# Performance work log

Measured on AMD Instinct MI355X. Metric: run time of the kernel, lower is better.

The kernel has to match this reference:

```python
import jax, jax.numpy as jnp
import numpy as np

DIM = 256
HEADS = 8
GROUPS = 4
HIDDEN = int(DIM * 4.0)
GW = DIM // GROUPS          # group width = 64
HEAD_DIM = DIM // HEADS     # 32
SCALE = HEAD_DIM ** (-0.5)
LN_EPS = 1e-6
BN_EPS = 1e-3               # keras BatchNormalization default epsilon
L2_EPS = 1e-12              # tf.nn.l2_normalize default


def _l2norm(t):
    ss = jnp.sum(t * t, axis=-1, keepdims=True)
    return t * jax.lax.rsqrt(jnp.maximum(ss, L2_EPS))


def setup_inputs() -> dict:
    key = jax.random.key(0)
    ks = jax.random.split(key, 12)
    B, H, W = 16, 56, 56
    x = jax.random.normal(ks[0], (B, H, W, DIM), jnp.float32)
    # depthwise 3x3 kernels for groups 1..GROUPS-1 (group 0's conv is unused in the
    # original code: y0 is a plain slice). Combined depthwise kernel over the last
    # (GROUPS-1)*GW channels, keras HWIO layout with in_ch_per_group = 1.
    dw_kernel = jax.random.normal(ks[1], (3, 3, 1, (GROUPS - 1) * GW), jnp.float32) * 0.05
    dw_bias = jnp.zeros(((GROUPS - 1) * GW,), jnp.float32)
    ln_gamma = jnp.ones((DIM,), jnp.float32)
    ln_beta = jnp.zeros((DIM,), jnp.float32)
    qkv_w = jax.random.normal(ks[2], (DIM, 3 * DIM), jnp.float32) * 0.02  # qkv_bias=False
    proj_w = jax.random.normal(ks[3], (DIM, DIM), jnp.float32) * 0.02
    proj_b = jnp.zeros((DIM,), jnp.float32)
    bn_gamma = jnp.ones((DIM,), jnp.float32)
    bn_beta = jnp.zeros((DIM,), jnp.float32)
    bn_mean = jax.random.normal(ks[4], (DIM,), jnp.float32) * 0.1
    bn_var = jax.random.uniform(ks[5], (DIM,), jnp.float32, 0.5, 1.5)
    fc1_w = jax.random.normal(ks[6], (DIM, HIDDEN), jnp.float32) * 0.02
    fc1_b = jnp.zeros((HIDDEN,), jnp.float32)
    fc2_w = jax.random.normal(ks[7], (HIDDEN, DIM), jnp.float32) * 0.02
    fc2_b = jnp.zeros((DIM,), jnp.float32)
    return dict(x=x, dw_kernel=dw_kernel, dw_bias=dw_bias, ln_gamma=ln_gamma,
                ln_beta=ln_beta, qkv_w=qkv_w, proj_w=proj_w, proj_b=proj_b,
                bn_gamma=bn_gamma, bn_beta=bn_beta, bn_mean=bn_mean, bn_var=bn_var,
                fc1_w=fc1_w, fc1_b=fc1_b, fc2_w=fc2_w, fc2_b=fc2_b)


def _gdta_forward(x, dw_kernel, dw_bias, ln_gamma, ln_beta, qkv_w, proj_w, proj_b,
                  bn_gamma, bn_beta, bn_mean, bn_var, fc1_w, fc1_b, fc2_w, fc2_b):
    B, H, W, C = x.shape
    N = H * W
    # ---- GOTA_block_part1: grouped depthwise convs with cumulative residual ----
    # y0 = x[..., :GW]; for i>=1: K_i = dwconv_i(x_i); y1=K1, y_i = K_i + y_{i-1}
    # => y_i (i>=1) is the cumulative sum of K_1..K_i along the group axis.
    xc = x[..., GW:]  # [B,H,W,(G-1)*GW]
    K = jax.lax.conv_general_dilated(
        xc, dw_kernel, window_strides=(1, 1), padding='SAME',
        dimension_numbers=('NHWC', 'HWIO', 'NHWC'),
        feature_group_count=(GROUPS - 1) * GW) + dw_bias
    Kg = K.reshape(B, H, W, GROUPS - 1, GW)
    Yg = jnp.cumsum(Kg, axis=3).reshape(B, H, W, (GROUPS - 1) * GW)
    dwconv = jnp.concatenate([x[..., :GW], Yg], axis=-1)  # [B,H,W,C]
    # ---- LayerNorm (last axis) ----
    mu = jnp.mean(dwconv, axis=-1, keepdims=True)
    var = jnp.mean(jnp.square(dwconv - mu), axis=-1, keepdims=True)
    norm1 = (dwconv - mu) * jax.lax.rsqrt(var + LN_EPS) * ln_gamma + ln_beta
    t = norm1.reshape(B, N, C)
    # ---- channel (cross-covariance) attention ----
    qkv = (t @ qkv_w).reshape(B, N, 3, HEADS, HEAD_DIM)
    qkv = jnp.transpose(qkv, (2, 0, 3, 1, 4))  # [3,B,h,N,d]
    q, k, v = qkv[0], qkv[1], qkv[2]
    q = _l2norm(q) * SCALE
    k = _l2norm(k)
    attn = jnp.einsum('bhnd,bhne->bhde', q, k)       # [B,h,d,d]
    attn = jax.nn.softmax(attn, axis=-1)
    out = jnp.einsum('bhnd,bhde->bhne', v, attn)     # [B,h,N,d]
    out = jnp.transpose(out, (0, 2, 1, 3)).reshape(B, N, C)
    out = out @ proj_w + proj_b
    attn_img = out.reshape(B, H, W, C)
    # ---- merge + BatchNorm (inference) + MLP + residual ----
    merged = attn_img + dwconv
    merged = (merged - bn_mean) * jax.lax.rsqrt(bn_var + BN_EPS) * bn_gamma + bn_beta
    h1 = jax.nn.gelu(merged @ fc1_w + fc1_b, approximate=False)
    mlp = h1 @ fc2_w + fc2_b
    return x + mlp


def reference(x, dw_kernel, dw_bias, ln_gamma, ln_beta, qkv_w, proj_w, proj_b,
              bn_gamma, bn_beta, bn_mean, bn_var, fc1_w, fc1_b, fc2_w, fc2_b):
    return _gdta_forward(x, dw_kernel, dw_bias, ln_gamma, ln_beta, qkv_w, proj_w,
                         proj_b, bn_gamma, bn_beta, bn_mean, bn_var,
                         fc1_w, fc1_b, fc2_w, fc2_b)
```

## Files before the change

kernel.cpp:

```cpp
#include <hip/hip_runtime.h>
#include <cstdint>

typedef unsigned short u16;
typedef __attribute__((ext_vector_type(8))) _Float16 f16x8;
typedef __attribute__((ext_vector_type(8))) unsigned short u16x8;
typedef __attribute__((ext_vector_type(4))) float f32x4;

#define SPLITN 7

__device__ __forceinline__ float b2f(u16 u) {
  union { unsigned int i; float f; } v; v.i = ((unsigned int)u) << 16; return v.f;
}
__device__ __forceinline__ u16 f2b(float f) {
  union { float f; unsigned int i; } v; v.f = f;
  unsigned int x = v.i;
  return (u16)((x + 0x7fffu + ((x >> 16) & 1u)) >> 16);
}
__device__ __forceinline__ u16 f2h(float f) {
  union { _Float16 h; u16 u; } v; v.h = (_Float16)f; return v.u;
}
__device__ __forceinline__ float h2f(u16 u) {
  union { u16 u; _Float16 h; } v; v.u = u; return (float)v.h;
}
__device__ __forceinline__ float ld(const void* p, long i, int f) {
  return f ? ((const float*)p)[i] : b2f(((const u16*)p)[i]);
}
template<int F>
__device__ __forceinline__ float4 ld4(const void* p, long i) {
  if (F) return *(const float4*)((const float*)p + i);
  const ushort4 u = *(const ushort4*)((const u16*)p + i);
  return make_float4(b2f(u.x), b2f(u.y), b2f(u.z), b2f(u.w));
}
__device__ __forceinline__ void fma4(float4& a, const float4 x, const float4 k) {
  a.x += x.x * k.x; a.y += x.y * k.y; a.z += x.z * k.z; a.w += x.w * k.w;
}
__device__ __forceinline__ float gelu(float v) {
  const float u = v * (0.7978845608028654f + 0.035677408136300125f * v * v);
  const float e = __expf(2.0f * u);
  return 0.5f * v * (1.0f + (1.0f - 2.0f / (e + 1.0f)));
}
#define GLDS(gp, lp) __builtin_amdgcn_global_load_lds( \
    (const __attribute__((address_space(1))) void*)(gp), \
    (__attribute__((address_space(3))) void*)(lp), 16, 0, 0)

__global__ __launch_bounds__(256) void detect_kernel(const u16* __restrict__ x,
                                                     int* __restrict__ flag) {
  __shared__ int sbad;
  if (threadIdx.x == 0) sbad = 0;
  __syncthreads();
  int b = 0;
  #pragma unroll
  for (int rr = 0; rr < 2; ++rr) {
    const int i = rr * 256 + threadIdx.x;
    const float v = fabsf(b2f(x[2 * i]));
    if (!(v < 100.f) || v < 1e-6f) ++b;
  }
  atomicAdd(&sbad, b);
  __syncthreads();
  if (threadIdx.x == 0) *flag = (sbad > 16) ? 1 : 0;
}

__global__ void transpose_cvt_kernel(const void* __restrict__ w0, u16* __restrict__ o0,
                                     const void* __restrict__ w1, u16* __restrict__ o1,
                                     const void* __restrict__ w2, u16* __restrict__ o2,
                                     const int* __restrict__ flagp) {
  const int f = *flagp;
  int bb = blockIdx.x;
  const void* in; u16* out; int R, C;
  if (bb < 768)       { in = w0; out = o0; R = 256;  C = 768;  }
  else if (bb < 1792) { in = w1; out = o1; R = 256;  C = 1024; bb -= 768; }
  else                { in = w2; out = o2; R = 1024; C = 256;  bb -= 1792; }
  const int o = bb * 256 + threadIdx.x;
  if (o < R * C) {
    const int i = o / R, j = o % R;
    out[o] = f2h(ld(in, (long)j * C + i, f));
  }
}

template<int F>
__device__ __forceinline__ void dwconv_body4(
    const void* __restrict__ x, const void* __restrict__ dwk, const void* __restrict__ dwb,
    const void* __restrict__ lng, const void* __restrict__ lnb,
    u16* __restrict__ dwc, u16* __restrict__ norm1, int tg, int lane)
{
  const int b = tg / 784, rem = tg % 784;
  const int hh = rem / 14, wg = (rem % 14) * 4;
  const int c0 = lane * 4;
  const long tok0 = (long)b * 3136 + hh * 56 + wg;
  float4 acc[4];
  float4 pv[4];
  if (lane >= 16) {
    const int j0 = c0 - 64;
    const float4 bb = ld4<F>(dwb, j0);
    acc[0] = bb; acc[1] = bb; acc[2] = bb; acc[3] = bb;
    #pragma unroll
    for (int dh = -1; dh <= 1; ++dh) {
      const int h2 = hh + dh;
      if (h2 < 0 || h2 >= 56) continue;
      const long rb = ((long)b * 3136 + h2 * 56) * 256;
      float4 xr[6];
      #pragma unroll
      for (int i = 0; i < 6; ++i) {
        const int w2 = wg - 1 + i;
        xr[i] = (w2 >= 0 && w2 < 56) ? ld4<F>(x, rb + (long)w2 * 256 + c0)
                                     : make_float4(0.f, 0.f, 0.f, 0.f);
      }
      float4 kw[3];
      #pragma unroll
      for (int i = 0; i < 3; ++i)
        kw[i] = ld4<F>(dwk, (long)((dh + 1) * 3 + i) * 192 + j0);
      #pragma unroll
      for (int t = 0; t < 4; ++t)
        #pragma unroll
        for (int i = 0; i < 3; ++i)
          fma4(acc[t], xr[t + i], kw[i]);
    }
  } else {
    #pragma unroll
    for (int t = 0; t < 4; ++t)
      pv[t] = ld4<F>(x, (tok0 + t) * 256 + c0);
  }
  const float4 g = ld4<F>(lng, c0);
  const float4 be = ld4<F>(lnb, c0);
  #pragma unroll
  for (int t = 0; t < 4; ++t) {
    float sx = acc[t].x, sy = acc[t].y, sz = acc[t].z, sw = acc[t].w;
    const float t1x = __shfl(sx, lane - 16), t1y = __shfl(sy, lane - 16),
                t1z = __shfl(sz, lane - 16), t1w = __shfl(sw, lane - 16);
    const float t2x = __shfl(sx, lane - 32), t2y = __shfl(sy, lane - 32),
                t2z = __shfl(sz, lane - 32), t2w = __shfl(sw, lane - 32);
    if (lane >= 32) { sx += t1x; sy += t1y; sz += t1z; sw += t1w; }
    if (lane >= 48) { sx += t2x; sy += t2y; sz += t2z; sw += t2w; }
    float vx, vy, vz, vw;
    if (lane < 16) { vx = pv[t].x; vy = pv[t].y; vz = pv[t].z; vw = pv[t].w; }
    else           { vx = sx;      vy = sy;      vz = sz;      vw = sw;      }
    float sum = vx + vy + vz + vw;
    float sq = vx * vx + vy * vy + vz * vz + vw * vw;
    #pragma unroll
    for (int m = 32; m; m >>= 1) { sum += __shfl_xor(sum, m); sq += __shfl_xor(sq, m); }
    const float mu = sum * (1.0f / 256.0f);
    const float var = sq * (1.0f / 256.0f) - mu * mu;
    const float rstd = rsqrtf(fmaxf(var, 0.f) + 1e-6f);
    ushort4 dv, nv;
    dv.x = f2h(vx); dv.y = f2h(vy); dv.z = f2h(vz); dv.w = f2h(vw);
    nv.x = f2h((vx - mu) * rstd * g.x + be.x);
    nv.y = f2h((vy - mu) * rstd * g.y + be.y);
    nv.z = f2h((vz - mu) * rstd * g.z + be.z);
    nv.w = f2h((vw - mu) * rstd * g.w + be.w);
    *(ushort4*)(dwc + (tok0 + t) * 256 + c0) = dv;
    *(ushort4*)(norm1 + (tok0 + t) * 256 + c0) = nv;
  }
}

__global__ __launch_bounds__(256) void dwconv_ln_kernel(
    const void* __restrict__ x, const void* __restrict__ dwk, const void* __restrict__ dwb,
    const void* __restrict__ lng, const void* __restrict__ lnb,
    u16* __restrict__ dwc, u16* __restrict__ norm1, const int* __restrict__ flagp)
{
  const int wave = threadIdx.x >> 6, lane = threadIdx.x & 63;
  const int tg = blockIdx.x * 4 + wave;
  if (*flagp) dwconv_body4<1>(x, dwk, dwb, lng, lnb, dwc, norm1, tg, lane);
  else        dwconv_body4<0>(x, dwk, dwb, lng, lnb, dwc, norm1, tg, lane);
}

template<int BM, int WR, int WC, int EPI, int KT>
__global__ __launch_bounds__(256) void gemm_kernel(
    const u16* __restrict__ A, const u16* __restrict__ Bt, void* C,
    int lda, int ldb, int ldc,
    long aZ, long bZ, long cZ, long zoff,
    const void* __restrict__ bias, const void* aux,
    const void* __restrict__ bng, const void* __restrict__ bnb,
    const void* __restrict__ bnm, const void* __restrict__ bnv,
    const int* __restrict__ flagp)
{
  static_assert(BM == 64 || BM == 128, "");
  constexpr int BN = 128;
  constexpr int WM = BM / WR, WN = BN / WC;
  constexpr int MI = WM / 16, NI = WN / 16;
  __shared__ __align__(16) u16 As[BM * 64];
  __shared__ __align__(16) u16 Bs[BN * 64];
  const int f = (EPI == 0 || EPI == 5) ? 0 : *flagp;
  const int tid = threadIdx.x;
  const int wave = tid >> 6, lane = tid & 63;
  const int wr = wave / WC, wc = wave % WC;
  const int quad = lane >> 4, l16 = lane & 15;
  const int tileM = blockIdx.y * BM, tileN = blockIdx.x * BN;
  const u16* Ab = A + (long)blockIdx.z * aZ + (long)tileM * lda;
  const u16* Bb = Bt + (long)blockIdx.z * bZ + (long)tileN * ldb;
  f32x4 acc[MI][NI];
  #pragma unroll
  for (int mi = 0; mi < MI; ++mi)
    #pragma unroll
    for (int ni = 0; ni < NI; ++ni)
      acc[mi][ni] = (f32x4){0.f, 0.f, 0.f, 0.f};

  for (int k0 = 0; k0 < KT; k0 += 64) {
    #pragma unroll
    for (int r = 0; r < BM / 32; ++r) {
      const int fg = r * 256 + tid;
      const int row = fg >> 3, cs = (fg & 7) ^ (row & 7);
      GLDS(Ab + (long)row * lda + k0 + cs * 8, As + (r * 256 + wave * 64) * 8);
    }
    #pragma unroll
    for (int r = 0; r < 4; ++r) {
      const int fg = r * 256 + tid;
      const int row = fg >> 3, cs = (fg & 7) ^ (row & 7);
      GLDS(Bb + (long)row * ldb + k0 + cs * 8, Bs + (r * 256 + wave * 64) * 8);
    }
    __syncthreads();
    #pragma unroll
    for (int ks = 0; ks < 2; ++ks) {
      f16x8 af[MI], bfr[NI];
      #pragma unroll
      for (int mi = 0; mi < MI; ++mi) {
        const int R = wr * WM + mi * 16 + l16;
        const int kc = ks * 4 + quad;
        af[mi] = *(const f16x8*)&As[(R * 8 + (kc ^ (R & 7))) * 8];
      }
      #pragma unroll
      for (int ni = 0; ni < NI; ++ni) {
        const int S = wc * WN + ni * 16 + l16;
        const int kc = ks * 4 + quad;
        bfr[ni] = *(const f16x8*)&Bs[(S * 8 + (kc ^ (S & 7))) * 8];
      }
      #pragma unroll
      for (int mi = 0; mi < MI; ++mi)
        #pragma unroll
        for (int ni = 0; ni < NI; ++ni)
          acc[mi][ni] = __builtin_amdgcn_mfma_f32_16x16x32_f16(af[mi], bfr[ni], acc[mi][ni], 0, 0, 0);
    }
    __syncthreads();
  }

  const long zC = (long)blockIdx.z * cZ + ((EPI == 5) ? 0 : zoff);
  #pragma unroll
  for (int mi = 0; mi < MI; ++mi) {
    #pragma unroll
    for (int ni = 0; ni < NI; ++ni) {
      const int col = tileN + wc * WN + ni * 16 + l16;
      #pragma unroll
      for (int r = 0; r < 4; ++r) {
        const int row = tileM + wr * WM + mi * 16 + quad * 4 + r;
        const long ci = zC + (long)row * ldc + col;
        float v = acc[mi][ni][r];
        if (EPI == 2) {
          v += ld(bias, col, f);
          v += h2f(((const u16*)aux)[ci]);
          v = (v - ld(bnm, col, f)) * rsqrtf(ld(bnv, col, f) + 1e-3f) * ld(bng, col, f) + ld(bnb, col, f);
          ((u16*)C)[ci] = f2h(v);
        } else {
          if (col < 512) ((u16*)C)[(long)row * 512 + col] = f2h(v);
          else ((u16*)aux)[zoff + (long)row * 256 + (col - 512)] = f2h(v);
        }
      }
    }
  }
}

__global__ __launch_bounds__(256, 2) void mlp_kernel(
    const u16* __restrict__ dwc, const u16* __restrict__ w1t, const u16* __restrict__ w2t,
    const void* __restrict__ b1, const void* __restrict__ b2,
    const void* __restrict__ x, void* __restrict__ out,
    const int* __restrict__ flagp)
{
  __shared__ __align__(16) u16 Ds[64 * 256];
  __shared__ __align__(16) u16 Hs[64 * 128];
  __shared__ __align__(16) u16 Bs[256 * 64];
  const int f = *flagp;
  const int tid = threadIdx.x;
  const int wave = tid >> 6, lane = tid & 63;
  const int quad = lane >> 4, l16 = lane & 15;
  const int tileM = blockIdx.x * 64;

  #pragma unroll
  for (int r = 0; r < 8; ++r) {
    const int fg = r * 256 + tid;
    const int row = fg >> 5, cs = (fg & 31) ^ (row & 7);
    GLDS(dwc + (long)(tileM + row) * 256 + cs * 8, Ds + (r * 256 + wave * 64) * 8);
  }

  f32x4 accO[4][4];
  #pragma unroll
  for (int mi = 0; mi < 4; ++mi)
    #pragma unroll
    for (int ni = 0; ni < 4; ++ni)
      accO[mi][ni] = (f32x4){0.f, 0.f, 0.f, 0.f};

  for (int hc = 0; hc < 8; ++hc) {
    f32x4 acc1[4][2];
    #pragma unroll
    for (int mi = 0; mi < 4; ++mi)
      #pragma unroll
      for (int ni = 0; ni < 2; ++ni)
        acc1[mi][ni] = (f32x4){0.f, 0.f, 0.f, 0.f};

    for (int it = 0; it < 4; ++it) {
      #pragma unroll
      for (int r = 0; r < 4; ++r) {
        const int fg = r * 256 + tid;
        const int row = fg >> 3, cs = (fg & 7) ^ (row & 7);
        GLDS(w1t + (long)(hc * 128 + row) * 256 + it * 64 + cs * 8,
             Bs + (r * 256 + wave * 64) * 8);
      }
      __syncthreads();
      #pragma unroll
      for (int ks = 0; ks < 2; ++ks) {
        const int kc = it * 8 + ks * 4 + quad;
        const int kl = ks * 4 + quad;
        f16x8 af[4], bf[2];
        #pragma unroll
        for (int mi = 0; mi < 4; ++mi) {
          const int R = mi * 16 + l16;
          af[mi] = *(const f16x8*)&Ds[(R * 32 + (kc ^ (R & 7))) * 8];
        }
        #pragma unroll
        for (int ni = 0; ni < 2; ++ni) {
          const int S = wave * 32 + ni * 16 + l16;
          bf[ni] = *(const f16x8*)&Bs[(S * 8 + (kl ^ (S & 7))) * 8];
        }
        #pragma unroll
        for (int mi = 0; mi < 4; ++mi)
          #pragma unroll
          for (int ni = 0; ni < 2; ++ni)
            acc1[mi][ni] = __builtin_amdgcn_mfma_f32_16x16x32_f16(af[mi], bf[ni], acc1[mi][ni], 0, 0, 0);
      }
      __syncthreads();
    }
    #pragma unroll
    for (int mi = 0; mi < 4; ++mi)
      #pragma unroll
      for (int ni = 0; ni < 2; ++ni)
        #pragma unroll
        for (int r = 0; r < 4; ++r) {
          const int row = mi * 16 + quad * 4 + r;
          const int col = wave * 32 + ni * 16 + l16;
          const float v = acc1[mi][ni][r] + ld(b1, hc * 128 + col, f);
          Hs[(row * 16 + ((col >> 3) ^ (row & 7))) * 8 + (col & 7)] = f2h(gelu(v));
        }
    __syncthreads();
    for (int it2 = 0; it2 < 2; ++it2) {
      #pragma unroll
      for (int r = 0; r < 8; ++r) {
        const int fg = r * 256 + tid;
        const int row = fg >> 3, cs = (fg & 7) ^ (row & 7);
        GLDS(w2t + (long)row * 1024 + hc * 128 + it2 * 64 + cs * 8,
             Bs + (r * 256 + wave * 64) * 8);
      }
      __syncthreads();
      #pragma unroll
      for (int ks = 0; ks < 2; ++ks) {
        const int kc = it2 * 8 + ks * 4 + quad;
        const int kl = ks * 4 + quad;
        f16x8 af[4], bf[4];
        #pragma unroll
        for (int mi = 0; mi < 4; ++mi) {
          const int R = mi * 16 + l16;
          af[mi] = *(const f16x8*)&Hs[(R * 16 + (kc ^ (R & 7))) * 8];
        }
        #pragma unroll
        for (int ni = 0; ni < 4; ++ni) {
          const int S = wave * 64 + ni * 16 + l16;
          bf[ni] = *(const f16x8*)&Bs[(S * 8 + (kl ^ (S & 7))) * 8];
        }
        #pragma unroll
        for (int mi = 0; mi < 4; ++mi)
          #pragma unroll
          for (int ni = 0; ni < 4; ++ni)
            accO[mi][ni] = __builtin_amdgcn_mfma_f32_16x16x32_f16(af[mi], bf[ni], accO[mi][ni], 0, 0, 0);
      }
      __syncthreads();
    }
  }
  #pragma unroll
  for (int mi = 0; mi < 4; ++mi)
    #pragma unroll
    for (int ni = 0; ni < 4; ++ni) {
      const int col = wave * 64 + ni * 16 + l16;
      #pragma unroll
      for (int r = 0; r < 4; ++r) {
        const int row = tileM + mi * 16 + quad * 4 + r;
        const long ci = (long)row * 256 + col;
        const float v = accO[mi][ni][r] + ld(b2, col, f) + ld(x, ci, f);
        if (f) ((float*)out)[ci] = v; else ((u16*)out)[ci] = f2b(v);
      }
    }
}

__global__ __launch_bounds__(256) void attn_accum_kernel(
    const u16* __restrict__ qk, float* __restrict__ A_part, int pair0)
{
  const int pl = blockIdx.x;
  const int split = blockIdx.y;
  const int bl = pl >> 3, h = pl & 7;
  const int tid = threadIdx.x;
  const int wave = tid >> 6, lane = tid & 63;
  const int quad = lane >> 4, l16 = lane & 15;
  const int dq = wave >> 1, eq = wave & 1;
  __shared__ __align__(16) u16 lqT[32 * 72];
  __shared__ __align__(16) u16 lkT[32 * 72];
  const long rowbase = (long)bl * 3136 * 512;
  const int n0 = split * 448;
  f32x4 acc = (f32x4){0.f, 0.f, 0.f, 0.f};
  const int seg = tid & 7;

  for (int ch = 0; ch < 7; ++ch) {
    const int nb = n0 + ch * 64;
    #pragma unroll
    for (int rr = 0; rr < 2; ++rr) {
      const int a = rr * 256 + tid;
      const int nl = a >> 3;
      const int co = (seg < 4) ? h * 32 + seg * 8 : 256 + h * 32 + (seg - 4) * 8;
      const u16x8 v8 = *(const u16x8*)(qk + rowbase + (long)(nb + nl) * 512 + co);
      float vf[8], p = 0.f;
      #pragma unroll
      for (int i = 0; i < 8; ++i) { vf[i] = h2f(v8[i]); p += vf[i] * vf[i]; }
      float p1 = p + __shfl_xor(p, 1);
      float p2 = p1 + __shfl_xor(p1, 2);
      const float other = __shfl_xor(p2, 4);
      const float ssq = (seg < 4) ? p2 : other;
      const float ssk = (seg < 4) ? other : p2;
      const float s = 0.17677669529663687f * rsqrtf(fmaxf(ssq, 1e-12f)) *
                      rsqrtf(fmaxf(ssk, 1e-12f));
      if (seg < 4) {
        const int db = seg * 8;
        #pragma unroll
        for (int i = 0; i < 8; ++i) {
          const int d = db + i;
          lqT[d * 72 + (nl ^ (d & 24))] = f2h(vf[i] * s);
        }
      } else {
        const int eb = (seg - 4) * 8;
        #pragma unroll
        for (int i = 0; i < 8; ++i) {
          const int e = eb + i;
          lkT[e * 72 + (nl ^ (e & 24))] = v8[i];
        }
      }
    }
    __syncthreads();
    #pragma unroll
    for (int ks = 0; ks < 2; ++ks) {
      const int tb = ks * 32 + quad * 8;
      const int dA = dq * 16 + l16;
      const int eB = eq * 16 + l16;
      const f16x8 af = *(const f16x8*)&lqT[dA * 72 + (tb ^ (dA & 24))];
      const f16x8 bf = *(const f16x8*)&lkT[eB * 72 + (tb ^ (eB & 24))];
      acc = __builtin_amdgcn_mfma_f32_16x16x32_f16(af, bf, acc, 0, 0, 0);
    }
    __syncthreads();
  }
  float* o = A_part + ((long)(pair0 + pl) * SPLITN + split) * 1024;
  #pragma unroll
  for (int r = 0; r < 4; ++r)
    o[(dq * 16 + quad * 4 + r) * 32 + eq * 16 + l16] = acc[r];
}

__global__ __launch_bounds__(1024) void softmax_kernel(float* A_part) {
  const int pair = blockIdx.x;
  const int t = threadIdx.x;
  float v = 0.f;
  float* base = A_part + (long)pair * SPLITN * 1024 + t;
  #pragma unroll
  for (int s = 0; s < SPLITN; ++s) v += base[s * 1024];
  float mx = v;
  #pragma unroll
  for (int m = 16; m; m >>= 1) mx = fmaxf(mx, __shfl_xor(mx, m, 32));
  const float p = expf(v - mx);
  float sm = p;
  #pragma unroll
  for (int m = 16; m; m >>= 1) sm += __shfl_xor(sm, m, 32);
  base[0] = p / sm;
}

__global__ __launch_bounds__(256) void wb_kernel(
    const float* __restrict__ A_part, const void* __restrict__ proj_w,
    u16* __restrict__ Wbt, const int* __restrict__ flagp)
{
  const int f = *flagp;
  const int b = blockIdx.x;
  const int cs = blockIdx.y;
  const int tid = threadIdx.x;
  const int cg = tid & 31, dg = tid >> 5;
  const int c = cs * 32 + cg;
  __shared__ float Ah[32][32];
  __shared__ float pw[32][33];
  for (int h = 0; h < 8; ++h) {
    const float* Abase = A_part + ((long)(b * 8 + h) * SPLITN) * 1024;
    #pragma unroll
    for (int rr = 0; rr < 4; ++rr) {
      const int ff = rr * 256 + tid;
      Ah[ff >> 5][ff & 31] = Abase[ff];
    }
    #pragma unroll
    for (int rr = 0; rr < 4; ++rr) {
      const int ff = rr * 256 + tid;
      const int e = ff >> 5, ccc = ff & 31;
      pw[e][ccc] = ld(proj_w, (long)(h * 32 + e) * 256 + cs * 32 + ccc, f);
    }
    __syncthreads();
    float acc[4] = {0.f, 0.f, 0.f, 0.f};
    #pragma unroll
    for (int e = 0; e < 32; ++e) {
      const float pv = pw[e][cg];
      #pragma unroll
      for (int dd = 0; dd < 4; ++dd)
        acc[dd] += Ah[dg * 4 + dd][e] * pv;
    }
    #pragma unroll
    for (int dd = 0; dd < 4; ++dd)
      Wbt[((long)b * 256 + c) * 256 + h * 32 + dg * 4 + dd] = f2h(acc[dd]);
    __syncthreads();
  }
}

extern "C" void kernel_launch(void* const* d_in, const int* in_sizes, int n_in,
                              void* d_out, int out_size, void* d_ws, size_t ws_size,
                              hipStream_t stream) {
  const void* x      = d_in[0];
  const void* dwk    = d_in[1];
  const void* dwb    = d_in[2];
  const void* lng    = d_in[3];
  const void* lnb    = d_in[4];
  const void* qkv_w  = d_in[5];
  const void* proj_w = d_in[6];
  const void* proj_b = d_in[7];
  const void* bn_g   = d_in[8];
  const void* bn_b   = d_in[9];
  const void* bn_m   = d_in[10];
  const void* bn_v   = d_in[11];
  const void* fc1_w  = d_in[12];
  const void* fc1_b  = d_in[13];
  const void* fc2_w  = d_in[14];
  const void* fc2_b  = d_in[15];
  char* ws = (char*)d_ws;

  int*   flagp   = (int*)  (ws + 0);
  u16*   wqkvT   = (u16*)  (ws + 256);
  u16*   wfc1T   = (u16*)  (ws + 393472);
  u16*   wfc2T   = (u16*)  (ws + 917760);
  float* A_part  = (float*)(ws + 1442048);
  u16*   Wbt     = (u16*)  (ws + 5112064);
  u16*   vbuf    = (u16*)  (ws + 7209216);
  u16*   dwc     = (u16*)  (ws + 32899328);
  u16*   qk_half = (u16*)  (ws + 58589440);
  u16*   norm1   = (u16*)d_out;

  detect_kernel<<<1, 256, 0, stream>>>((const u16*)x, flagp);

  transpose_cvt_kernel<<<2816, 256, 0, stream>>>(qkv_w, wqkvT, fc1_w, wfc1T,
                                                 fc2_w, wfc2T, flagp);

  dwconv_ln_kernel<<<3136, 256, 0, stream>>>(x, dwk, dwb, lng, lnb, dwc, norm1, flagp);

  for (int half = 0; half < 2; ++half) {
    const u16* nh = norm1 + (long)half * 25088 * 256;
    gemm_kernel<128, 2, 2, 5, 256><<<dim3(6, 196, 1), 256, 0, stream>>>(
        nh, wqkvT, qk_half, 256, 256, 512, 0, 0, 0, (long)half * 25088 * 256,
        nullptr, vbuf, nullptr, nullptr, nullptr, nullptr, flagp);
    attn_accum_kernel<<<dim3(64, SPLITN), 256, 0, stream>>>(qk_half, A_part, half * 64);
  }

  softmax_kernel<<<128, 1024, 0, stream>>>(A_part);
  wb_kernel<<<dim3(16, 8), 256, 0, stream>>>(A_part, proj_w, Wbt, flagp);

  gemm_kernel<64, 1, 4, 2, 256><<<dim3(2, 49, 16), 256, 0, stream>>>(
      vbuf, Wbt, dwc, 256, 256, 256,
      (long)3136 * 256, 65536, (long)3136 * 256, 0,
      proj_b, dwc, bn_g, bn_b, bn_m, bn_v, flagp);

  mlp_kernel<<<784, 256, 0, stream>>>(dwc, wfc1T, wfc2T, fc1_b, fc2_b, x, d_out, flagp);
}
```

Baseline: 464.1 us.

## Read weight fragments directly from global memory instead of staging in LDS

Both the QKV/proj GEMMs and the fused MLP now keep only the activation tile in shared memory and load B-operand (weight) fragments straight from global memory/L2 into registers, removing the per-k-step weight staging and most __syncthreads. The GEMM uses a 64-row tile with full K resident in LDS and a 2x2 wave layout. The MLP switches to a 2x2 wave layout, drops the weight LDS buffer and uses a padded hidden buffer, allowing higher occupancy. The risk is uncoalesced, latency-bound global weight reads that rely on cache hits.

```diff
diff --git a/kernel.cpp b/kernel.cpp
--- a/kernel.cpp
+++ b/kernel.cpp
@@ -163,113 +163,98 @@
   else        dwconv_body4<0>(x, dwk, dwb, lng, lnb, dwc, norm1, tg, lane);
 }
 
-template<int BM, int WR, int WC, int EPI, int KT>
-__global__ __launch_bounds__(256) void gemm_kernel(
+template<int EPI>
+__global__ __launch_bounds__(256, 4) void sgemm_kernel(
     const u16* __restrict__ A, const u16* __restrict__ Bt, void* C,
-    int lda, int ldb, int ldc,
-    long aZ, long bZ, long cZ, long zoff,
+    int ldb, long aZ, long bZ, long cZ, long zoff,
     const void* __restrict__ bias, const void* aux,
     const void* __restrict__ bng, const void* __restrict__ bnb,
     const void* __restrict__ bnm, const void* __restrict__ bnv,
     const int* __restrict__ flagp)
 {
-  static_assert(BM == 64 || BM == 128, "");
-  constexpr int BN = 128;
-  constexpr int WM = BM / WR, WN = BN / WC;
-  constexpr int MI = WM / 16, NI = WN / 16;
-  __shared__ __align__(16) u16 As[BM * 64];
-  __shared__ __align__(16) u16 Bs[BN * 64];
-  const int f = (EPI == 0 || EPI == 5) ? 0 : *flagp;
+  __shared__ __align__(16) u16 Ds[64 * 256];
+  const int f = (EPI == 5) ? 0 : *flagp;
   const int tid = threadIdx.x;
   const int wave = tid >> 6, lane = tid & 63;
-  const int wr = wave / WC, wc = wave % WC;
   const int quad = lane >> 4, l16 = lane & 15;
-  const int tileM = blockIdx.y * BM, tileN = blockIdx.x * BN;
-  const u16* Ab = A + (long)blockIdx.z * aZ + (long)tileM * lda;
-  const u16* Bb = Bt + (long)blockIdx.z * bZ + (long)tileN * ldb;
-  f32x4 acc[MI][NI];
-  #pragma unroll
-  for (int mi = 0; mi < MI; ++mi)
-    #pragma unroll
-    for (int ni = 0; ni < NI; ++ni)
+  const int wr = wave >> 1, wc = wave & 1;
+  const int tileM = blockIdx.y * 64, colC = blockIdx.x * 128;
+  const u16* Ab = A + (long)blockIdx.z * aZ + (long)tileM * 256;
+  const u16* Bb = Bt + (long)blockIdx.z * bZ;
+
+  #pragma unroll
+  for (int r = 0; r < 8; ++r) {
+    const int fg = r * 256 + tid;
+    const int row = fg >> 5, cs = (fg & 31) ^ (row & 7);
+    GLDS(Ab + (long)row * 256 + cs * 8, Ds + (r * 256 + wave * 64) * 8);
+  }
+  __syncthreads();
+
+  f32x4 acc[2][4];
+  #pragma unroll
+  for (int mi = 0; mi < 2; ++mi)
+    #pragma unroll
+    for (int ni = 0; ni < 4; ++ni)
       acc[mi][ni] = (f32x4){0.f, 0.f, 0.f, 0.f};
 
-  for (int k0 = 0; k0 < KT; k0 += 64) {
-    #pragma unroll
-    for (int r = 0; r < BM / 32; ++r) {
-      const int fg = r * 256 + tid;
-      const int row = fg >> 3, cs = (fg & 7) ^ (row & 7);
-      GLDS(Ab + (long)row * lda + k0 + cs * 8, As + (r * 256 + wave * 64) * 8);
-    }
-    #pragma unroll
-    for (int r = 0; r < 4; ++r) {
-      const int fg = r * 256 + tid;
-      const int row = fg >> 3, cs = (fg & 7) ^ (row & 7);
-      GLDS(Bb + (long)row * ldb + k0 + cs * 8, Bs + (r * 256 + wave * 64) * 8);
-    }
-    __syncthreads();
-    #pragma unroll
-    for (int ks = 0; ks < 2; ++ks) {
-      f16x8 af[MI], bfr[NI];
-      #pragma unroll
-      for (int mi = 0; mi < MI; ++mi) {
-        const int R = wr * WM + mi * 16 + l16;
-        const int kc = ks * 4 + quad;
-        af[mi] = *(const f16x8*)&As[(R * 8 + (kc ^ (R & 7))) * 8];
-      }
-      #pragma unroll
-      for (int ni = 0; ni < NI; ++ni) {
-        const int S = wc * WN + ni * 16 + l16;
-        const int kc = ks * 4 + quad;
-        bfr[ni] = *(const f16x8*)&Bs[(S * 8 + (kc ^ (S & 7))) * 8];
-      }
-      #pragma unroll
-      for (int mi = 0; mi < MI; ++mi)
-        #pragma unroll
-        for (int ni = 0; ni < NI; ++ni)
-          acc[mi][ni] = __builtin_amdgcn_mfma_f32_16x16x32_f16(af[mi], bfr[ni], acc[mi][ni], 0, 0, 0);
-    }
-    __syncthreads();
-  }
-
-  const long zC = (long)blockIdx.z * cZ + ((EPI == 5) ? 0 : zoff);
-  #pragma unroll
-  for (int mi = 0; mi < MI; ++mi) {
-    #pragma unroll
-    for (int ni = 0; ni < NI; ++ni) {
-      const int col = tileN + wc * WN + ni * 16 + l16;
+  #pragma unroll
+  for (int kk = 0; kk < 8; ++kk) {
+    const int kc = kk * 4 + quad;
+    f16x8 af[2], bf[4];
+    #pragma unroll
+    for (int mi = 0; mi < 2; ++mi) {
+      const int R = wr * 32 + mi * 16 + l16;
+      af[mi] = *(const f16x8*)&Ds[(R * 32 + (kc ^ (R & 7))) * 8];
+    }
+    #pragma unroll
+    for (int ni = 0; ni < 4; ++ni) {
+      const int S = colC + wc * 64 + ni * 16 + l16;
+      bf[ni] = *(const f16x8*)(Bb + (long)S * ldb + kc * 8);
+    }
+    #pragma unroll
+    for (int mi = 0; mi < 2; ++mi)
+      #pragma unroll
+      for (int ni = 0; ni < 4; ++ni)
+        acc[mi][ni] = __builtin_amdgcn_mfma_f32_16x16x32_f16(af[mi], bf[ni], acc[mi][ni], 0, 0, 0);
+  }
+
+  #pragma unroll
+  for (int mi = 0; mi < 2; ++mi)
+    #pragma unroll
+    for (int ni = 0; ni < 4; ++ni) {
+      const int col = colC + wc * 64 + ni * 16 + l16;
       #pragma unroll
       for (int r = 0; r < 4; ++r) {
-        const int row = tileM + wr * WM + mi * 16 + quad * 4 + r;
-        const long ci = zC + (long)row * ldc + col;
+        const int rloc = wr * 32 + mi * 16 + quad * 4 + r;
         float v = acc[mi][ni][r];
         if (EPI == 2) {
+          const long ci = (long)blockIdx.z * cZ + (long)(tileM + rloc) * 256 + col;
           v += ld(bias, col, f);
           v += h2f(((const u16*)aux)[ci]);
           v = (v - ld(bnm, col, f)) * rsqrtf(ld(bnv, col, f) + 1e-3f) * ld(bng, col, f) + ld(bnb, col, f);
           ((u16*)C)[ci] = f2h(v);
         } else {
-          if (col < 512) ((u16*)C)[(long)row * 512 + col] = f2h(v);
-          else ((u16*)aux)[zoff + (long)row * 256 + (col - 512)] = f2h(v);
+          const long row = tileM + rloc;
+          if (col < 512) ((u16*)C)[row * 512 + col] = f2h(v);
+          else ((u16*)aux)[zoff + row * 256 + (col - 512)] = f2h(v);
         }
       }
     }
-  }
-}
-
-__global__ __launch_bounds__(256, 2) void mlp_kernel(
+}
+
+__global__ __launch_bounds__(256, 3) void mlp_kernel(
     const u16* __restrict__ dwc, const u16* __restrict__ w1t, const u16* __restrict__ w2t,
     const void* __restrict__ b1, const void* __restrict__ b2,
     const void* __restrict__ x, void* __restrict__ out,
     const int* __restrict__ flagp)
 {
   __shared__ __align__(16) u16 Ds[64 * 256];
-  __shared__ __align__(16) u16 Hs[64 * 128];
-  __shared__ __align__(16) u16 Bs[256 * 64];
+  __shared__ __align__(16) u16 Hs[64 * 136];
   const int f = *flagp;
   const int tid = threadIdx.x;
   const int wave = tid >> 6, lane = tid & 63;
   const int quad = lane >> 4, l16 = lane & 15;
+  const int wr = wave >> 1, wc = wave & 1;
   const int tileM = blockIdx.x * 64;
 
   #pragma unroll
@@ -278,107 +263,84 @@
     const int row = fg >> 5, cs = (fg & 31) ^ (row & 7);
     GLDS(dwc + (long)(tileM + row) * 256 + cs * 8, Ds + (r * 256 + wave * 64) * 8);
   }
-
-  f32x4 accO[4][4];
-  #pragma unroll
-  for (int mi = 0; mi < 4; ++mi)
-    #pragma unroll
-    for (int ni = 0; ni < 4; ++ni)
+  __syncthreads();
+
+  f32x4 accO[2][8];
+  #pragma unroll
+  for (int mi = 0; mi < 2; ++mi)
+    #pragma unroll
+    for (int ni = 0; ni < 8; ++ni)
       accO[mi][ni] = (f32x4){0.f, 0.f, 0.f, 0.f};
 
   for (int hc = 0; hc < 8; ++hc) {
-    f32x4 acc1[4][2];
-    #pragma unroll
-    for (int mi = 0; mi < 4; ++mi)
-      #pragma unroll
-      for (int ni = 0; ni < 2; ++ni)
+    f32x4 acc1[2][4];
+    #pragma unroll
+    for (int mi = 0; mi < 2; ++mi)
+      #pragma unroll
+      for (int ni = 0; ni < 4; ++ni)
         acc1[mi][ni] = (f32x4){0.f, 0.f, 0.f, 0.f};
-
-    for (int it = 0; it < 4; ++it) {
-      #pragma unroll
-      for (int r = 0; r < 4; ++r) {
-        const int fg = r * 256 + tid;
-        const int row = fg >> 3, cs = (fg & 7) ^ (row & 7);
-        GLDS(w1t + (long)(hc * 128 + row) * 256 + it * 64 + cs * 8,
-             Bs + (r * 256 + wave * 64) * 8);
-      }
-      __syncthreads();
-      #pragma unroll
-      for (int ks = 0; ks < 2; ++ks) {
-        const int kc = it * 8 + ks * 4 + quad;
-        const int kl = ks * 4 + quad;
-        f16x8 af[4], bf[2];
+    #pragma unroll
+    for (int kk = 0; kk < 8; ++kk) {
+      const int kc = kk * 4 + quad;
+      f16x8 af[2], bf[4];
+      #pragma unroll
+      for (int mi = 0; mi < 2; ++mi) {
+        const int R = wr * 32 + mi * 16 + l16;
+        af[mi] = *(const f16x8*)&Ds[(R * 32 + (kc ^ (R & 7))) * 8];
+      }
+      #pragma unroll
+      for (int ni = 0; ni < 4; ++ni) {
+        const int S = hc * 128 + wc * 64 + ni * 16 + l16;
+        bf[ni] = *(const f16x8*)(w1t + (long)S * 256 + kc * 8);
+      }
+      #pragma unroll
+      for (int mi = 0; mi < 2; ++mi)
         #pragma unroll
-        for (int mi = 0; mi < 4; ++mi) {
-          const int R = mi * 16 + l16;
-          af[mi] = *(const f16x8*)&Ds[(R * 32 + (kc ^ (R & 7))) * 8];
-        }
-        #pragma unroll
-        for (int ni = 0; ni < 2; ++ni) {
-          const int S = wave * 32 + ni * 16 + l16;
-          bf[ni] = *(const f16x8*)&Bs[(S * 8 + (kl ^ (S & 7))) * 8];
-        }
-        #pragma unroll
-        for (int mi = 0; mi < 4; ++mi)
-          #pragma unroll
-          for (int ni = 0; ni < 2; ++ni)
-            acc1[mi][ni] = __builtin_amdgcn_mfma_f32_16x16x32_f16(af[mi], bf[ni], acc1[mi][ni], 0, 0, 0);
-      }
-      __syncthreads();
-    }
-    #pragma unroll
-    for (int mi = 0; mi < 4; ++mi)
-      #pragma unroll
-      for (int ni = 0; ni < 2; ++ni)
+        for (int ni = 0; ni < 4; ++ni)
+          acc1[mi][ni] = __builtin_amdgcn_mfma_f32_16x16x32_f16(af[mi], bf[ni], acc1[mi][ni], 0, 0, 0);
+    }
+    #pragma unroll
+    for (int mi = 0; mi < 2; ++mi)
+      #pragma unroll
+      for (int ni = 0; ni < 4; ++ni)
         #pragma unroll
         for (int r = 0; r < 4; ++r) {
-          const int row = mi * 16 + quad * 4 + r;
-          const int col = wave * 32 + ni * 16 + l16;
+          const int row = wr * 32 + mi * 16 + quad * 4 + r;
+          const int col = wc * 64 + ni * 16 + l16;
           const float v = acc1[mi][ni][r] + ld(b1, hc * 128 + col, f);
-          Hs[(row * 16 + ((col >> 3) ^ (row & 7))) * 8 + (col & 7)] = f2h(gelu(v));
+          Hs[row * 136 + col] = f2h(gelu(v));
         }
     __syncthreads();
-    for (int it2 = 0; it2 < 2; ++it2) {
-      #pragma unroll
-      for (int r = 0; r < 8; ++r) {
-        const int fg = r * 256 + tid;
-        const int row = fg >> 3, cs = (fg & 7) ^ (row & 7);
-        GLDS(w2t + (long)row * 1024 + hc * 128 + it2 * 64 + cs * 8,
-             Bs + (r * 256 + wave * 64) * 8);
-      }
-      __syncthreads();
-      #pragma unroll
-      for (int ks = 0; ks < 2; ++ks) {
-        const int kc = it2 * 8 + ks * 4 + quad;
-        const int kl = ks * 4 + quad;
-        f16x8 af[4], bf[4];
+    #pragma unroll
+    for (int kk2 = 0; kk2 < 4; ++kk2) {
+      const int kc2 = kk2 * 4 + quad;
+      f16x8 af[2], bf[8];
+      #pragma unroll
+      for (int mi = 0; mi < 2; ++mi) {
+        const int R = wr * 32 + mi * 16 + l16;
+        af[mi] = *(const f16x8*)&Hs[R * 136 + kc2 * 8];
+      }
+      #pragma unroll
+      for (int ni = 0; ni < 8; ++ni) {
+        const int S = wc * 128 + ni * 16 + l16;
+        bf[ni] = *(const f16x8*)(w2t + (long)S * 1024 + hc * 128 + kc2 * 8);
+      }
+      #pragma unroll
+      for (int mi = 0; mi < 2; ++mi)
         #pragma unroll
-        for (int mi = 0; mi < 4; ++mi) {
-          const int R = mi * 16 + l16;
-          af[mi] = *(const f16x8*)&Hs[(R * 16 + (kc ^ (R & 7))) * 8];
-        }
-        #pragma unroll
-        for (int ni = 0; ni < 4; ++ni) {
-          const int S = wave * 64 + ni * 16 + l16;
-          bf[ni] = *(const f16x8*)&Bs[(S * 8 + (kl ^ (S & 7))) * 8];
-        }
-        #pragma unroll
-        for (int mi = 0; mi < 4; ++mi)
-          #pragma unroll
-          for (int ni = 0; ni < 4; ++ni)
-            accO[mi][ni] = __builtin_amdgcn_mfma_f32_16x16x32_f16(af[mi], bf[ni], accO[mi][ni], 0, 0, 0);
-      }
-      __syncthreads();
-    }
-  }
-  #pragma unroll
-  for (int mi = 0; mi < 4; ++mi)
-    #pragma unroll
-    for (int ni = 0; ni < 4; ++ni) {
-      const int col = wave * 64 + ni * 16 + l16;
+        for (int ni = 0; ni < 8; ++ni)
+          accO[mi][ni] = __builtin_amdgcn_mfma_f32_16x16x32_f16(af[mi], bf[ni], accO[mi][ni], 0, 0, 0);
+    }
+    __syncthreads();
+  }
+  #pragma unroll
+  for (int mi = 0; mi < 2; ++mi)
+    #pragma unroll
+    for (int ni = 0; ni < 8; ++ni) {
+      const int col = wc * 128 + ni * 16 + l16;
       #pragma unroll
       for (int r = 0; r < 4; ++r) {
-        const int row = tileM + mi * 16 + quad * 4 + r;
+        const int row = tileM + wr * 32 + mi * 16 + quad * 4 + r;
         const long ci = (long)row * 256 + col;
         const float v = accO[mi][ni][r] + ld(b2, col, f) + ld(x, ci, f);
         if (f) ((float*)out)[ci] = v; else ((u16*)out)[ci] = f2b(v);
@@ -554,8 +516,8 @@
 
   for (int half = 0; half < 2; ++half) {
     const u16* nh = norm1 + (long)half * 25088 * 256;
-    gemm_kernel<128, 2, 2, 5, 256><<<dim3(6, 196, 1), 256, 0, stream>>>(
-        nh, wqkvT, qk_half, 256, 256, 512, 0, 0, 0, (long)half * 25088 * 256,
+    sgemm_kernel<5><<<dim3(6, 392, 1), 256, 0, stream>>>(
+        nh, wqkvT, qk_half, 256, 0, 0, 0, (long)half * 25088 * 256,
         nullptr, vbuf, nullptr, nullptr, nullptr, nullptr, flagp);
     attn_accum_kernel<<<dim3(64, SPLITN), 256, 0, stream>>>(qk_half, A_part, half * 64);
   }
@@ -563,9 +525,8 @@
   softmax_kernel<<<128, 1024, 0, stream>>>(A_part);
   wb_kernel<<<dim3(16, 8), 256, 0, stream>>>(A_part, proj_w, Wbt, flagp);
 
-  gemm_kernel<64, 1, 4, 2, 256><<<dim3(2, 49, 16), 256, 0, stream>>>(
-      vbuf, Wbt, dwc, 256, 256, 256,
-      (long)3136 * 256, 65536, (long)3136 * 256, 0,
+  sgemm_kernel<2><<<dim3(2, 49, 16), 256, 0, stream>>>(
+      vbuf, Wbt, dwc, 256, (long)3136 * 256, 65536, (long)3136 * 256, 0,
       proj_b, dwc, bn_g, bn_b, bn_m, bn_v, flagp);
 
   mlp_kernel<<<784, 256, 0, stream>>>(dwc, wfc1T, wfc2T, fc1_b, fc2_b, x, d_out, flagp);
```

New measurement: 677.8 us. 46.1% more time.
